# Kernel tuning notes

Hardware: AMD Instinct MI355X
Metric: run time of the kernel (lower is better)

The kernel has to match this reference:

```python
import jax, jax.numpy as jnp
import numpy as np


def setup_inputs() -> dict:
    key = jax.random.key(0)
    k1, k2, k3 = jax.random.split(key, 3)
    B, L, H = 4, 4096, 1024
    x = jax.random.normal(k1, (B, L, H), dtype=jnp.float32)
    # 0.02 scale keeps attention logits in a sane range (like trained weights)
    in_proj_weight = jax.random.normal(k2, (3 * H, H), dtype=jnp.float32) * 0.02
    in_proj_bias = jnp.zeros((3 * H,), dtype=jnp.float32)
    out_proj_weight = jax.random.normal(k3, (H, H), dtype=jnp.float32) * 0.02
    out_proj_bias = jnp.zeros((H,), dtype=jnp.float32)
    return {
        "x": x,
        "in_proj_weight": in_proj_weight,
        "in_proj_bias": in_proj_bias,
        "out_proj_weight": out_proj_weight,
        "out_proj_bias": out_proj_bias,
        "num_heads": 16,
        "window_size": 128,
    }


def _windowed_mha(x, in_proj_weight, in_proj_bias, out_proj_weight, out_proj_bias,
                  num_heads, window_size):
    B, L, H = x.shape
    P = window_size
    pad = (-L) % P  # static
    xp = jnp.pad(x, ((0, 0), (0, pad), (0, 0))) if pad else x
    Lp = xp.shape[1]
    nw = Lp // P
    w = xp.reshape(B * nw, P, H)  # [NW, P, H]
    # packed QKV projection (torch MHA: q,k,v = split(x @ W_in.T + b_in))
    qkv = jnp.einsum('nph,dh->npd', w, in_proj_weight) + in_proj_bias
    q, k, v = jnp.split(qkv, 3, axis=-1)
    hd = H // num_heads

    def to_heads(t):
        return t.reshape(B * nw, P, num_heads, hd).transpose(0, 2, 1, 3)  # [NW, Hh, P, hd]

    q, k, v = to_heads(q), to_heads(k), to_heads(v)
    scale = 1.0 / jnp.sqrt(jnp.asarray(hd, dtype=x.dtype))
    scores = jnp.einsum('nhqd,nhkd->nhqk', q * scale, k)  # [NW, Hh, P, P]
    attn = jax.nn.softmax(scores, axis=-1)
    o = jnp.einsum('nhqk,nhkd->nhqd', attn, v)  # [NW, Hh, P, hd]
    o = o.transpose(0, 2, 1, 3).reshape(B * nw, P, H)
    o = jnp.einsum('nph,oh->npo', o, out_proj_weight) + out_proj_bias
    o = o.reshape(B, Lp, H)
    return o[:, :L]


def reference(x, in_proj_weight, in_proj_bias, out_proj_weight, out_proj_bias,
              num_heads, window_size):
    return _windowed_mha(x, in_proj_weight, in_proj_bias, out_proj_weight,
                         out_proj_bias, num_heads, window_size)
```

## Files before the change

kernel.cpp:

```cpp
#include <hip/hip_runtime.h>
#include <hip/hip_bf16.h>
#include <cstdint>


typedef __bf16 bf16_t;
typedef __bf16 bf16x8 __attribute__((ext_vector_type(8)));
typedef __bf16 bf16x4 __attribute__((ext_vector_type(4)));
typedef float  floatx4 __attribute__((ext_vector_type(4)));

#define MFMA_16x16x32(A, B, C) __builtin_amdgcn_mfma_f32_16x16x32_bf16(A, B, C, 0, 0, 0)

__device__ __forceinline__ void gld_lds16(const bf16_t* g, bf16_t* l) {
  __builtin_amdgcn_global_load_lds(
      (__attribute__((address_space(1))) void*)(void*)(g),
      (__attribute__((address_space(3))) void*)(l), 16, 0, 0);
}

__device__ __forceinline__ void cvt8(const float* __restrict__ s,
                                     bf16_t* __restrict__ d) {
  float4 a = ((const float4*)s)[0];
  float4 b = ((const float4*)s)[1];
  bf16x8 o;
  o[0] = (bf16_t)a.x; o[1] = (bf16_t)a.y; o[2] = (bf16_t)a.z; o[3] = (bf16_t)a.w;
  o[4] = (bf16_t)b.x; o[5] = (bf16_t)b.y; o[6] = (bf16_t)b.z; o[7] = (bf16_t)b.w;
  *(bf16x8*)d = o;
}

__global__ void cvt_w(const float* __restrict__ Win,
                      const float* __restrict__ Wout,
                      bf16_t* __restrict__ Wpk,
                      bf16_t* __restrict__ Woutb) {
  const int idx = blockIdx.x * 256 + threadIdx.x;
  if (idx < 131072) {
    cvt8(Wout + (size_t)idx * 8, Woutb + (size_t)idx * 8);
  } else {
    const int c = idx - 131072;
    const int dr = c >> 7, i = c & 127;
    const int head = dr / 192, s = dr - head * 192;
    const int src = (s < 64) ? head * 64 + s
                  : (s < 128) ? 1024 + head * 64 + (s - 64)
                              : 2048 + head * 64 + (s - 128);
    cvt8(Win + (size_t)src * 1024 + i * 8, Wpk + (size_t)dr * 1024 + i * 8);
  }
}

__global__ __launch_bounds__(256, 2) void gemm_out(
    const bf16_t* __restrict__ A, const bf16_t* __restrict__ Bm,
    const float* __restrict__ bias, float* __restrict__ C,
    int M, int N, int K) {
  __shared__ bf16_t As[128 * 64];
  __shared__ bf16_t Bs[256 * 64];
  const int tid  = threadIdx.x;
  const int lane = tid & 63;
  const int wave = tid >> 6;
  const int n16  = lane & 15;
  const int q4   = lane >> 4;
  const int wm   = (wave >> 1) * 64;
  const int wn   = (wave & 1) * 128;
  const int m0   = blockIdx.y * 128;
  const int n0   = blockIdx.x * 256;

  floatx4 acc[4][8] = {};

  for (int k0 = 0; k0 < K; k0 += 64) {
    __syncthreads();
#pragma unroll
    for (int it = 0; it < 4; ++it) {
      const int ch = it * 256 + tid;
      const int r  = ch >> 3;
      const int c8 = (ch & 7) ^ (r & 7);
      gld_lds16(A + (size_t)(m0 + r) * K + k0 + c8 * 8,
                As + (it * 256 + wave * 64) * 8);
    }
#pragma unroll
    for (int it = 0; it < 8; ++it) {
      const int ch = it * 256 + tid;
      const int r  = ch >> 3;
      const int c8 = (ch & 7) ^ (r & 7);
      gld_lds16(Bm + (size_t)(n0 + r) * K + k0 + c8 * 8,
                Bs + (it * 256 + wave * 64) * 8);
    }
    __syncthreads();

#pragma unroll
    for (int half = 0; half < 2; ++half) {
      bf16x8 af[4], bfr[8];
#pragma unroll
      for (int i = 0; i < 4; ++i) {
        const int row = wm + i * 16 + n16;
        af[i] = *(const bf16x8*)&As[row * 64 + (((half * 4 + q4) ^ (row & 7)) * 8)];
      }
#pragma unroll
      for (int j = 0; j < 8; ++j) {
        const int row = wn + j * 16 + n16;
        bfr[j] = *(const bf16x8*)&Bs[row * 64 + (((half * 4 + q4) ^ (row & 7)) * 8)];
      }
#pragma unroll
      for (int i = 0; i < 4; ++i)
#pragma unroll
        for (int j = 0; j < 8; ++j)
          acc[i][j] = MFMA_16x16x32(af[i], bfr[j], acc[i][j]);
    }
  }

#pragma unroll
  for (int i = 0; i < 4; ++i)
#pragma unroll
    for (int j = 0; j < 8; ++j) {
      const int col = n0 + wn + j * 16 + n16;
      const float b = bias[col];
#pragma unroll
      for (int r = 0; r < 4; ++r) {
        const int row = m0 + wm + i * 16 + q4 * 4 + r;
        C[(size_t)row * N + col] = acc[i][j][r] + b;
      }
    }
}

__global__ __launch_bounds__(256, 3) void qkv_attn(
    const float* __restrict__ Xf,
    const bf16_t* __restrict__ Wpk,
    const float* __restrict__ bin,
    bf16_t* __restrict__ o)
{
  __shared__ bf16_t smem[26624];
  bf16_t* Xs  = smem;
  bf16_t* Ws  = smem + 8192;
  bf16_t* qs  = smem;
  bf16_t* ks  = smem + 9216;
  bf16_t* vsT = smem + 18432;
  bf16_t* Ps  = smem;

  const int wid  = blockIdx.x;
  const int h    = blockIdx.y;
  const int tid  = threadIdx.x;
  const int lane = tid & 63;
  const int wave = tid >> 6;
  const int n16  = lane & 15;
  const int q4   = lane >> 4;
  const int wm   = (wave >> 1) * 64;
  const int wn   = (wave & 1) * 96;

  const float*  Xg = Xf + (size_t)wid * 128 * 1024;
  const bf16_t* Wg = Wpk + (size_t)h * 192 * 1024;

  floatx4 acc[4][6] = {};
  for (int k0 = 0; k0 < 1024; k0 += 64) {
    __syncthreads();
    float4 xa[4], xb_[4];
#pragma unroll
    for (int it = 0; it < 4; ++it) {
      const int ch = it * 256 + tid;
      const int r  = ch >> 3;
      const int c8 = (ch & 7) ^ (r & 7);
      const float4* src = (const float4*)(Xg + (size_t)r * 1024 + k0 + c8 * 8);
      xa[it]  = src[0];
      xb_[it] = src[1];
    }
#pragma unroll
    for (int it = 0; it < 6; ++it) {
      const int ch = it * 256 + tid;
      const int r  = ch >> 3;
      const int c8 = (ch & 7) ^ (r & 7);
      gld_lds16(Wg + (size_t)r * 1024 + k0 + c8 * 8,
                Ws + (it * 256 + wave * 64) * 8);
    }
#pragma unroll
    for (int it = 0; it < 4; ++it) {
      const int ch = it * 256 + tid;
      bf16x8 v;
      v[0] = (bf16_t)xa[it].x;  v[1] = (bf16_t)xa[it].y;
      v[2] = (bf16_t)xa[it].z;  v[3] = (bf16_t)xa[it].w;
      v[4] = (bf16_t)xb_[it].x; v[5] = (bf16_t)xb_[it].y;
      v[6] = (bf16_t)xb_[it].z; v[7] = (bf16_t)xb_[it].w;
      *(bf16x8*)&Xs[ch * 8] = v;
    }
    __syncthreads();

#pragma unroll
    for (int half = 0; half < 2; ++half) {
      bf16x8 af[4], bfr[6];
#pragma unroll
      for (int i = 0; i < 4; ++i) {
        const int row = wm + i * 16 + n16;
        af[i] = *(const bf16x8*)&Xs[row * 64 + (((half * 4 + q4) ^ (row & 7)) * 8)];
      }
#pragma unroll
      for (int j = 0; j < 6; ++j) {
        const int row = wn + j * 16 + n16;
        bfr[j] = *(const bf16x8*)&Ws[row * 64 + (((half * 4 + q4) ^ (row & 7)) * 8)];
      }
#pragma unroll
      for (int i = 0; i < 4; ++i)
#pragma unroll
        for (int j = 0; j < 6; ++j)
          acc[i][j] = MFMA_16x16x32(af[i], bfr[j], acc[i][j]);
    }
  }
  __syncthreads();

#pragma unroll
  for (int j = 0; j < 6; ++j) {
    const int base = wn + j * 16;
    const int col  = base + n16;
    const int gb = (base < 64) ? h * 64 + col
                 : (base < 128) ? 1024 + h * 64 + (col - 64)
                                : 2048 + h * 64 + (col - 128);
    const float bias = bin[gb];
#pragma unroll
    for (int i = 0; i < 4; ++i) {
      const int row0 = wm + i * 16 + q4 * 4;
      if (base < 64) {
#pragma unroll
        for (int r = 0; r < 4; ++r)
          qs[(row0 + r) * 72 + col] = (bf16_t)((acc[i][j][r] + bias) * 0.125f);
      } else if (base < 128) {
#pragma unroll
        for (int r = 0; r < 4; ++r)
          ks[(row0 + r) * 72 + (col - 64)] = (bf16_t)(acc[i][j][r] + bias);
      } else {
        bf16x4 pv;
#pragma unroll
        for (int r = 0; r < 4; ++r) pv[r] = (bf16_t)(acc[i][j][r] + bias);
        const int d = col - 128;
        const int c8 = row0 >> 3, pos = row0 & 7;
        *(bf16x4*)&vsT[d * 128 + ((c8 ^ n16) << 3) + pos] = pv;
      }
    }
  }
  __syncthreads();

  floatx4 sacc[2][8] = {};
#pragma unroll
  for (int ks0 = 0; ks0 < 2; ++ks0) {
    bf16x8 aq[2];
#pragma unroll
    for (int i = 0; i < 2; ++i)
      aq[i] = *(const bf16x8*)&qs[(wave * 32 + i * 16 + n16) * 72 + ks0 * 32 + q4 * 8];
#pragma unroll
    for (int j = 0; j < 8; ++j) {
      bf16x8 bk = *(const bf16x8*)&ks[(j * 16 + n16) * 72 + ks0 * 32 + q4 * 8];
      sacc[0][j] = MFMA_16x16x32(aq[0], bk, sacc[0][j]);
      sacc[1][j] = MFMA_16x16x32(aq[1], bk, sacc[1][j]);
    }
  }
  __syncthreads();

  float invs[2][4];
#pragma unroll
  for (int i = 0; i < 2; ++i) {
#pragma unroll
    for (int r = 0; r < 4; ++r) {
      float vals[8];
      float s = 0.f;
#pragma unroll
      for (int j = 0; j < 8; ++j) {
        vals[j] = __expf(sacc[i][j][r]);
        s += vals[j];
      }
      for (int m = 1; m < 16; m <<= 1) s += __shfl_xor(s, m, 64);
      invs[i][r] = 1.0f / s;
      const int prow = wave * 32 + i * 16 + q4 * 4 + r;
#pragma unroll
      for (int j = 0; j < 8; ++j)
        Ps[prow * 136 + j * 16 + n16] = (bf16_t)vals[j];
    }
  }
  __syncthreads();

  floatx4 oacc[2][4] = {};
#pragma unroll
  for (int kk = 0; kk < 4; ++kk) {
    bf16x8 ap[2];
#pragma unroll
    for (int i = 0; i < 2; ++i)
      ap[i] = *(const bf16x8*)&Ps[(wave * 32 + i * 16 + n16) * 136 + kk * 32 + q4 * 8];
#pragma unroll
    for (int j = 0; j < 4; ++j) {
      const int d = j * 16 + n16;
      bf16x8 bv = *(const bf16x8*)&vsT[d * 128 + (((kk * 4 + q4) ^ n16) << 3)];
      oacc[0][j] = MFMA_16x16x32(ap[0], bv, oacc[0][j]);
      oacc[1][j] = MFMA_16x16x32(ap[1], bv, oacc[1][j]);
    }
  }

  bf16_t* go = o + (size_t)wid * 128 * 1024 + h * 64;
#pragma unroll
  for (int i = 0; i < 2; ++i)
#pragma unroll
    for (int j = 0; j < 4; ++j)
#pragma unroll
      for (int r = 0; r < 4; ++r) {
        const int row = wave * 32 + i * 16 + q4 * 4 + r;
        go[(size_t)row * 1024 + j * 16 + n16] = (bf16_t)(oacc[i][j][r] * invs[i][r]);
      }
}

extern "C" void kernel_launch(void* const* d_in, const int* in_sizes, int n_in,
                              void* d_out, int out_size, void* d_ws, size_t ws_size,
                              hipStream_t stream) {
  const float* x    = (const float*)d_in[0];
  const float* Win  = (const float*)d_in[1];
  const float* bin  = (const float*)d_in[2];
  const float* Wout = (const float*)d_in[3];
  const float* bout = (const float*)d_in[4];
  float* out = (float*)d_out;

  const size_t M = 16384, H = 1024, H3 = 3072;

  bf16_t* Wpk   = (bf16_t*)d_ws;
  bf16_t* Woutb = Wpk + H3 * H;
  bf16_t* ob    = Woutb + H * H;

  cvt_w<<<dim3(2048), 256, 0, stream>>>(Win, Wout, Wpk, Woutb);

  qkv_attn<<<dim3(128, 16), 256, 0, stream>>>(x, Wpk, bin, ob);

  gemm_out<<<dim3((unsigned)(H / 256), (unsigned)(M / 128)), 256, 0, stream>>>(
      ob, Woutb, bout, out, (int)M, (int)H, (int)H);
}
```

Before: 290.7 us.

## Software-pipeline X tile loads in QKV GEMM and split attention launch

Moves the fp32 X tile global loads one iteration ahead so the next tile's loads overlap the current MFMA work. Replaces __syncthreads with manual s_barrier plus explicit waitcnt that leaves the prefetched X loads outstanding. Also splits the qkv_attn grid into two launches over window halves via a base offset. This costs more live registers and an extra kernel launch.

Measured after the change: 438.0 us. 50.6% more time.

```diff
diff --git a/kernel.cpp b/kernel.cpp
--- a/kernel.cpp
+++ b/kernel.cpp
@@ -121,7 +121,8 @@
     const float* __restrict__ Xf,
     const bf16_t* __restrict__ Wpk,
     const float* __restrict__ bin,
-    bf16_t* __restrict__ o)
+    bf16_t* __restrict__ o,
+    int wbase)
 {
   __shared__ bf16_t smem[26624];
   bf16_t* Xs  = smem;
@@ -131,7 +132,7 @@
   bf16_t* vsT = smem + 18432;
   bf16_t* Ps  = smem;
 
-  const int wid  = blockIdx.x;
+  const int wid  = wbase + blockIdx.x;
   const int h    = blockIdx.y;
   const int tid  = threadIdx.x;
   const int lane = tid & 63;
@@ -145,18 +146,20 @@
   const bf16_t* Wg = Wpk + (size_t)h * 192 * 1024;
 
   floatx4 acc[4][6] = {};
+  float4 xa[4], xb_[4];
+#pragma unroll
+  for (int it = 0; it < 4; ++it) {
+    const int ch = it * 256 + tid;
+    const int r  = ch >> 3;
+    const int c8 = (ch & 7) ^ (r & 7);
+    const float4* src = (const float4*)(Xg + (size_t)r * 1024 + c8 * 8);
+    xa[it]  = src[0];
+    xb_[it] = src[1];
+  }
+
   for (int k0 = 0; k0 < 1024; k0 += 64) {
-    __syncthreads();
-    float4 xa[4], xb_[4];
-#pragma unroll
-    for (int it = 0; it < 4; ++it) {
-      const int ch = it * 256 + tid;
-      const int r  = ch >> 3;
-      const int c8 = (ch & 7) ^ (r & 7);
-      const float4* src = (const float4*)(Xg + (size_t)r * 1024 + k0 + c8 * 8);
-      xa[it]  = src[0];
-      xb_[it] = src[1];
-    }
+    __builtin_amdgcn_s_barrier();
+    __builtin_amdgcn_sched_barrier(0);
 #pragma unroll
     for (int it = 0; it < 6; ++it) {
       const int ch = it * 256 + tid;
@@ -165,6 +168,7 @@
       gld_lds16(Wg + (size_t)r * 1024 + k0 + c8 * 8,
                 Ws + (it * 256 + wave * 64) * 8);
     }
+    __builtin_amdgcn_sched_barrier(0);
 #pragma unroll
     for (int it = 0; it < 4; ++it) {
       const int ch = it * 256 + tid;
@@ -175,7 +179,25 @@
       v[6] = (bf16_t)xb_[it].z; v[7] = (bf16_t)xb_[it].w;
       *(bf16x8*)&Xs[ch * 8] = v;
     }
-    __syncthreads();
+    if (k0 + 64 < 1024) {
+#pragma unroll
+      for (int it = 0; it < 4; ++it) {
+        const int ch = it * 256 + tid;
+        const int r  = ch >> 3;
+        const int c8 = (ch & 7) ^ (r & 7);
+        const float4* src =
+            (const float4*)(Xg + (size_t)r * 1024 + (k0 + 64) + c8 * 8);
+        xa[it]  = src[0];
+        xb_[it] = src[1];
+      }
+      __builtin_amdgcn_sched_barrier(0);
+      asm volatile("s_waitcnt vmcnt(8) lgkmcnt(0)" ::: "memory");
+    } else {
+      __builtin_amdgcn_sched_barrier(0);
+      asm volatile("s_waitcnt vmcnt(0) lgkmcnt(0)" ::: "memory");
+    }
+    __builtin_amdgcn_s_barrier();
+    __builtin_amdgcn_sched_barrier(0);
 
 #pragma unroll
     for (int half = 0; half < 2; ++half) {
@@ -314,7 +336,8 @@
 
   cvt_w<<<dim3(2048), 256, 0, stream>>>(Win, Wout, Wpk, Woutb);
 
-  qkv_attn<<<dim3(128, 16), 256, 0, stream>>>(x, Wpk, bin, ob);
+  qkv_attn<<<dim3(64, 16), 256, 0, stream>>>(x, Wpk, bin, ob, 0);
+  qkv_attn<<<dim3(64, 16), 256, 0, stream>>>(x, Wpk, bin, ob, 64);
 
   gemm_out<<<dim3((unsigned)(H / 256), (unsigned)(M / 128)), 256, 0, stream>>>(
       ob, Woutb, bout, out, (int)M, (int)H, (int)H);
```

## Load X fragments directly from global into registers and remap blocks for XCD locality

Applied to the files above, without the earlier changes.

Removes the LDS staging of the fp32 input tile in the fused QKV+attention kernel. Each wave now loads its A-operand fragments straight from global memory and converts them to bf16 in registers, which saves LDS traffic and one conversion pass. The grid is flattened and remapped so that the 16 head-blocks of a window land on the same XCD, meant to improve L2 reuse of the shared X rows. The cost is that the two waves sharing the same rows (wn=0 and wn=96) now both read those rows from global/L2, and the loads are strided, less coalesced 32-byte reads per lane.

After: 515.1 us. 77.2% more time.

```diff
diff --git a/kernel.cpp b/kernel.cpp
--- a/kernel.cpp
+++ b/kernel.cpp
@@ -124,15 +124,17 @@
     bf16_t* __restrict__ o)
 {
   __shared__ bf16_t smem[26624];
-  bf16_t* Xs  = smem;
-  bf16_t* Ws  = smem + 8192;
+  bf16_t* Ws  = smem;
   bf16_t* qs  = smem;
   bf16_t* ks  = smem + 9216;
   bf16_t* vsT = smem + 18432;
   bf16_t* Ps  = smem;
 
-  const int wid  = blockIdx.x;
-  const int h    = blockIdx.y;
+  const int id   = blockIdx.x;
+  const int xcd  = id & 7;
+  const int t    = id >> 3;
+  const int h    = t & 15;
+  const int wid  = xcd + 8 * (t >> 4);
   const int tid  = threadIdx.x;
   const int lane = tid & 63;
   const int wave = tid >> 6;
@@ -147,16 +149,6 @@
   floatx4 acc[4][6] = {};
   for (int k0 = 0; k0 < 1024; k0 += 64) {
     __syncthreads();
-    float4 xa[4], xb_[4];
-#pragma unroll
-    for (int it = 0; it < 4; ++it) {
-      const int ch = it * 256 + tid;
-      const int r  = ch >> 3;
-      const int c8 = (ch & 7) ^ (r & 7);
-      const float4* src = (const float4*)(Xg + (size_t)r * 1024 + k0 + c8 * 8);
-      xa[it]  = src[0];
-      xb_[it] = src[1];
-    }
 #pragma unroll
     for (int it = 0; it < 6; ++it) {
       const int ch = it * 256 + tid;
@@ -165,30 +157,28 @@
       gld_lds16(Wg + (size_t)r * 1024 + k0 + c8 * 8,
                 Ws + (it * 256 + wave * 64) * 8);
     }
-#pragma unroll
-    for (int it = 0; it < 4; ++it) {
-      const int ch = it * 256 + tid;
-      bf16x8 v;
-      v[0] = (bf16_t)xa[it].x;  v[1] = (bf16_t)xa[it].y;
-      v[2] = (bf16_t)xa[it].z;  v[3] = (bf16_t)xa[it].w;
-      v[4] = (bf16_t)xb_[it].x; v[5] = (bf16_t)xb_[it].y;
-      v[6] = (bf16_t)xb_[it].z; v[7] = (bf16_t)xb_[it].w;
-      *(bf16x8*)&Xs[ch * 8] = v;
-    }
     __syncthreads();
 
 #pragma unroll
     for (int half = 0; half < 2; ++half) {
+      const int kq = half * 4 + q4;
       bf16x8 af[4], bfr[6];
 #pragma unroll
       for (int i = 0; i < 4; ++i) {
         const int row = wm + i * 16 + n16;
-        af[i] = *(const bf16x8*)&Xs[row * 64 + (((half * 4 + q4) ^ (row & 7)) * 8)];
+        const float4* xp = (const float4*)(Xg + (size_t)row * 1024 + k0 + kq * 8);
+        float4 lo = xp[0], hi = xp[1];
+        bf16x8 v;
+        v[0] = (bf16_t)lo.x; v[1] = (bf16_t)lo.y;
+        v[2] = (bf16_t)lo.z; v[3] = (bf16_t)lo.w;
+        v[4] = (bf16_t)hi.x; v[5] = (bf16_t)hi.y;
+        v[6] = (bf16_t)hi.z; v[7] = (bf16_t)hi.w;
+        af[i] = v;
       }
 #pragma unroll
       for (int j = 0; j < 6; ++j) {
         const int row = wn + j * 16 + n16;
-        bfr[j] = *(const bf16x8*)&Ws[row * 64 + (((half * 4 + q4) ^ (row & 7)) * 8)];
+        bfr[j] = *(const bf16x8*)&Ws[row * 64 + ((kq ^ (row & 7)) * 8)];
       }
 #pragma unroll
       for (int i = 0; i < 4; ++i)
@@ -314,7 +304,7 @@
 
   cvt_w<<<dim3(2048), 256, 0, stream>>>(Win, Wout, Wpk, Woutb);
 
-  qkv_attn<<<dim3(128, 16), 256, 0, stream>>>(x, Wpk, bin, ob);
+  qkv_attn<<<dim3(2048), 256, 0, stream>>>(x, Wpk, bin, ob);
 
   gemm_out<<<dim3((unsigned)(H / 256), (unsigned)(M / 128)), 256, 0, stream>>>(
       ob, Woutb, bout, out, (int)M, (int)H, (int)H);
```
